# Kernel tuning notes

Measured on AMD Instinct MI355X. Metric: run time of the kernel, lower is better.

## Reference

```python
import jax, jax.numpy as jnp
import numpy as np

B, S, D, H = 4, 2048, 1024, 16
HD = D // H  # 64

def setup_inputs() -> dict:
    key = jax.random.key(0)
    ks = jax.random.split(key, 6)
    scale = 1.0 / np.sqrt(D)
    return {
        "x": jax.random.normal(ks[0], (B, S, D), dtype=jnp.float32),
        "Wq": jax.random.normal(ks[1], (D, D), dtype=jnp.float32) * scale,
        "Wk": jax.random.normal(ks[2], (D, D), dtype=jnp.float32) * scale,
        "Wv": jax.random.normal(ks[3], (D, D), dtype=jnp.float32) * scale,
        "Wo": jax.random.normal(ks[4], (D, D), dtype=jnp.float32) * scale,
        "bo": jnp.zeros((D,), dtype=jnp.float32),
    }

def reference(x, Wq, Wk, Wv, Wo, bo):
    b, s, d = x.shape
    # projections (no bias for q/k/v, matching QKV_BIAS=False)
    q = (x @ Wq).reshape(b, s, H, HD).transpose(0, 2, 1, 3)  # [b,h,s,hd]
    k = (x @ Wk).reshape(b, s, H, HD).transpose(0, 2, 1, 3)
    v = (x @ Wv).reshape(b, s, H, HD).transpose(0, 2, 1, 3)
    scores = jnp.einsum('bhqd,bhkd->bhqk', q, k)  # [b,h,s,s]
    causal = jnp.tril(jnp.ones((s, s), dtype=bool))  # True where allowed
    scores = jnp.where(causal, scores, -jnp.inf)
    attn = jax.nn.softmax(scores / np.sqrt(HD), axis=-1)
    ctx = jnp.einsum('bhqk,bhkd->bhqd', attn, v)  # [b,h,s,hd]
    ctx = ctx.transpose(0, 2, 1, 3).reshape(b, s, d)
    return ctx @ Wo + bo
```

## Files before the change

### kernel.cpp

```cpp
#include <hip/hip_runtime.h>

#define BSZ 4
#define SEQ 2048
#define DIM 1024
#define NH  16
#define HD  64
#define QT  128
#define KT  64
#define PAD 72

typedef float v4f __attribute__((ext_vector_type(4)));
typedef short s8v __attribute__((ext_vector_type(8)));
typedef unsigned short u16;
typedef unsigned short u16x8 __attribute__((ext_vector_type(8)));
typedef unsigned short u16x4 __attribute__((ext_vector_type(4)));
typedef unsigned int u32;

__device__ __forceinline__ u16 f2bf(float f) {
  u32 u = __builtin_bit_cast(u32, f);
  u32 r = u + 0x7fffu + ((u >> 16) & 1u);
  return (u16)(r >> 16);
}
__device__ __forceinline__ float bf2f(u16 h) {
  return __builtin_bit_cast(float, (u32)h << 16);
}
__device__ __forceinline__ float fast_exp2(float x) {
#if __has_builtin(__builtin_amdgcn_exp2f)
  return __builtin_amdgcn_exp2f(x);
#else
  return exp2f(x);
#endif
}
__device__ __forceinline__ void gll16(const u16* g, u16* l) {
  __builtin_amdgcn_global_load_lds((const __attribute__((address_space(1))) void*)g,
                                   (__attribute__((address_space(3))) void*)l, 16, 0, 0);
}
__device__ __forceinline__ void wg_barrier() { asm volatile("s_barrier" ::: "memory"); }
#define WAITCNT_VM4 0xF74
#define WAITCNT_VM0 0xF70

__global__ __launch_bounds__(256) void cast_bf16_kernel(const float* __restrict__ x,
                                                        u16* __restrict__ o, int n4) {
  int i = blockIdx.x * 256 + threadIdx.x;
  if (i >= n4) return;
  v4f v = reinterpret_cast<const v4f*>(x)[i];
  u16x4 r;
  #pragma unroll
  for (int c = 0; c < 4; c++) r[c] = f2bf(v[c]);
  reinterpret_cast<u16x4*>(o)[i] = r;
}

__global__ __launch_bounds__(256) void transpose_cast_kernel(const float* __restrict__ W0,
                                                             const float* __restrict__ W1,
                                                             const float* __restrict__ W2,
                                                             const float* __restrict__ W3,
                                                             u16* __restrict__ out) {
  const float* W = blockIdx.z == 0 ? W0 : blockIdx.z == 1 ? W1 : blockIdx.z == 2 ? W2 : W3;
  const float scale = (blockIdx.z == 0) ? 0.18033688011112042f : 1.0f;
  u16* T = out + (size_t)blockIdx.z * DIM * DIM;
  __shared__ float tile[32][33];
  int tx = threadIdx.x & 31, ty = threadIdx.x >> 5;
  int bn = blockIdx.x * 32, bk = blockIdx.y * 32;
  #pragma unroll
  for (int r = 0; r < 4; r++) {
    int k = bk + ty + r * 8;
    tile[ty + r * 8][tx] = W[(size_t)k * DIM + bn + tx];
  }
  __syncthreads();
  #pragma unroll
  for (int r = 0; r < 4; r++) {
    int n = bn + ty + r * 8;
    T[(size_t)n * DIM + bk + tx] = f2bf(tile[tx][ty + r * 8] * scale);
  }
}


#define STAGE(s, kofs)                                                            \
  gll16(Ag0 + (kofs), Aw0 + (s) * 4096); gll16(Ag1 + (kofs), Aw1 + (s) * 4096);   \
  gll16(Bg0 + (kofs), Bw0 + (s) * 4096); gll16(Bg1 + (kofs), Bw1 + (s) * 4096);

#define COMPUTE(s)                                                                \
  { s8v af[4], bfv[4];                                                            \
    _Pragma("unroll") for (int i = 0; i < 4; i++)                                 \
      af[i] = *(const s8v*)(Al + (s) * 4096 + abase + i * 512);                   \
    _Pragma("unroll") for (int j = 0; j < 4; j++)                                 \
      bfv[j] = *(const s8v*)(Bl + (s) * 4096 + bbase + j * 512);                  \
    _Pragma("unroll") for (int i = 0; i < 4; i++)                                 \
      _Pragma("unroll") for (int j = 0; j < 4; j++)                               \
        acc[i][j] = __builtin_amdgcn_mfma_f32_16x16x32_bf16(af[i], bfv[j],        \
                                                            acc[i][j], 0, 0, 0); }

#define PIPE_STEP(s, nbuf, knext)                                                 \
  __builtin_amdgcn_s_waitcnt(WAITCNT_VM4);                                        \
  wg_barrier();                                                                   \
  STAGE(nbuf, knext)                                                              \
  COMPUTE(s)

#define GEMM_SETUP_AND_LOOP()                                                     \
  const int flat = blockIdx.x + 8 * blockIdx.y;                                   \
  const int xcd = flat & 7, slot = flat >> 3;                                     \
  const int m0 = (xcd * 8 + (slot & 7)) * 128;                                    \
  const int n0 = (slot >> 3) * 128;                                               \
  const int t = threadIdx.x;                                                      \
  const int lane = t & 63, w = t >> 6;                                            \
  const int waveM = w >> 1, waveN = w & 1;                                        \
  const int quad = lane >> 4, l16 = lane & 15;                                    \
  __shared__ u16 Al[12288];                                                       \
  __shared__ u16 Bl[12288];                                                       \
  v4f acc[4][4];                                                                  \
  _Pragma("unroll") for (int i = 0; i < 4; i++)                                   \
    _Pragma("unroll") for (int j = 0; j < 4; j++)                                 \
      acc[i][j] = (v4f){0.f, 0.f, 0.f, 0.f};                                      \
  const int sR = lane & 15, sC = lane >> 4;                                       \
  const u16* Ag0 = A  + (size_t)(m0 + (w * 2 + 0) * 16 + sR) * DIM + sC * 8;      \
  const u16* Ag1 = A  + (size_t)(m0 + (w * 2 + 1) * 16 + sR) * DIM + sC * 8;      \
  const u16* Bg0 = Bt + (size_t)(n0 + (w * 2 + 0) * 16 + sR) * DIM + sC * 8;      \
  const u16* Bg1 = Bt + (size_t)(n0 + (w * 2 + 1) * 16 + sR) * DIM + sC * 8;      \
  u16* Aw0 = Al + (w * 2 + 0) * 512;                                              \
  u16* Aw1 = Al + (w * 2 + 1) * 512;                                              \
  u16* Bw0 = Bl + (w * 2 + 0) * 512;                                              \
  u16* Bw1 = Bl + (w * 2 + 1) * 512;                                              \
  const int abase = waveM * 2048 + quad * 128 + l16 * 8;                          \
  const int bbase = waveN * 2048 + quad * 128 + l16 * 8;                          \
  STAGE(0, 0)                                                                     \
  STAGE(1, 32)                                                                    \
  for (int i3 = 0; i3 < 10; i3++) {                                               \
    const int kb = i3 * 96;                                                       \
    PIPE_STEP(0, 2, kb + 64)                                                      \
    PIPE_STEP(1, 0, kb + 96)                                                      \
    PIPE_STEP(2, 1, kb + 128)                                                     \
  }                                                                               \
  __builtin_amdgcn_s_waitcnt(WAITCNT_VM4);                                        \
  wg_barrier();                                                                   \
  COMPUTE(0)                                                                      \
  __builtin_amdgcn_s_waitcnt(WAITCNT_VM0);                                        \
  wg_barrier();                                                                   \
  COMPUTE(1)

__global__ __launch_bounds__(256, 3) void gemm_qkv(const u16* __restrict__ A, const u16* __restrict__ Wt,
                                                   u16* __restrict__ Qb, u16* __restrict__ Kb,
                                                   u16* __restrict__ Vtg) {
  const int z = blockIdx.z;
  const u16* Bt = Wt + (size_t)z * DIM * DIM;
  GEMM_SETUP_AND_LOOP()
  if (z == 2) {
    #pragma unroll
    for (int i = 0; i < 4; i++) {
      #pragma unroll
      for (int j = 0; j < 4; j++) {
        int gm0 = m0 + waveM * 64 + i * 16 + quad * 4;
        int gn = n0 + waveN * 64 + j * 16 + l16;
        int b = gm0 >> 11, s0 = gm0 & (SEQ - 1), hh = gn >> 6, d = gn & (HD - 1);
        u16x4 o;
        #pragma unroll
        for (int r = 0; r < 4; r++) o[r] = f2bf(acc[i][j][r]);
        *(u16x4*)(Vtg + ((size_t)(b * NH + hh) * HD + d) * SEQ + s0) = o;
      }
    }
  } else {
    u16* C = (z == 0) ? Qb : Kb;
    #pragma unroll
    for (int i = 0; i < 4; i++) {
      #pragma unroll
      for (int j = 0; j < 4; j++) {
        int gn = n0 + waveN * 64 + j * 16 + l16;
        #pragma unroll
        for (int r = 0; r < 4; r++) {
          int gm = m0 + waveM * 64 + i * 16 + quad * 4 + r;
          C[(size_t)gm * DIM + gn] = f2bf(acc[i][j][r]);
        }
      }
    }
  }
}

__global__ __launch_bounds__(256, 3) void gemm_proj(const u16* __restrict__ A, const u16* __restrict__ Bt,
                                                    float* __restrict__ Cf, const float* __restrict__ bias) {
  GEMM_SETUP_AND_LOOP()
  #pragma unroll
  for (int i = 0; i < 4; i++) {
    #pragma unroll
    for (int j = 0; j < 4; j++) {
      int gn = n0 + waveN * 64 + j * 16 + l16;
      float bv = bias[gn];
      #pragma unroll
      for (int r = 0; r < 4; r++) {
        int gm = m0 + waveM * 64 + i * 16 + quad * 4 + r;
        Cf[(size_t)gm * DIM + gn] = acc[i][j][r] + bv;
      }
    }
  }
}

__global__ __launch_bounds__(256, 3) void flash_attn_mfma(const u16* __restrict__ Qb,
                                                          const u16* __restrict__ Kb,
                                                          const u16* __restrict__ Vtg,
                                                          u16* __restrict__ Ob) {
  const int h = blockIdx.x, px = blockIdx.y, bb = blockIdx.z;
  const int t = threadIdx.x;
  const int lane = t & 63, w = t >> 6;
  const int quad = lane >> 4, l16 = lane & 15;

  __shared__ u16 QPs[QT * PAD];
  __shared__ u16 Ks[KT * PAD];
  __shared__ u16 Vs[HD * PAD];

  const size_t qkbase = (size_t)bb * SEQ * DIM + h * HD;
  const size_t vbase = ((size_t)bb * NH + h) * (size_t)HD * SEQ;

  const int vrow = t >> 2, scol = (t & 3) * 16;
  const int krow = ((vrow >> 5) + 2 * ((vrow >> 2) & 1)) * 16 + ((vrow >> 3) & 3) * 4 + (vrow & 3);

  for (int pass = 0; pass < 2; pass++) {
    const int qi = (pass == 0) ? px : (SEQ / QT - 1 - px);
    const int q0 = qi * QT;
    const int wq = q0 + w * 32;
    const int ntiles = 2 * qi + 2;

    __syncthreads();

    {
      const int r = t >> 1, c0 = (t & 1) * 32;
      const u16* src = Qb + qkbase + (size_t)(q0 + r) * DIM + c0;
      #pragma unroll
      for (int ch = 0; ch < 4; ch++)
        *(u16x8*)(QPs + r * PAD + c0 + ch * 8) = *(const u16x8*)(src + ch * 8);
    }
    __syncthreads();

    s8v qf[2][2];
    #pragma unroll
    for (int ni = 0; ni < 2; ni++)
      #pragma unroll
      for (int kc = 0; kc < 2; kc++)
        qf[ni][kc] = *(const s8v*)(QPs + (w * 32 + ni * 16 + l16) * PAD + kc * 32 + quad * 8);

    u16x8 kr0, kr1, vr0, vr1;
    {
      const u16* kp = Kb + qkbase + (size_t)vrow * DIM + scol;
      kr0 = *(const u16x8*)kp; kr1 = *(const u16x8*)(kp + 8);
      const u16* vp = Vtg + vbase + (size_t)vrow * SEQ + scol;
      vr0 = *(const u16x8*)vp; vr1 = *(const u16x8*)(vp + 8);
    }

    float mrun[2] = {-1e30f, -1e30f}, lrun[2] = {0.f, 0.f};
    v4f O[4][2];
    #pragma unroll
    for (int di = 0; di < 4; di++)
      #pragma unroll
      for (int ni = 0; ni < 2; ni++) O[di][ni] = (v4f){0.f, 0.f, 0.f, 0.f};

    for (int it = 0; it < ntiles; ++it) {
      const int kv0 = it * KT;
      __syncthreads();
      *(u16x8*)(Ks + krow * PAD + scol) = kr0;
      *(u16x8*)(Ks + krow * PAD + scol + 8) = kr1;
      *(u16x8*)(Vs + vrow * PAD + scol) = vr0;
      *(u16x8*)(Vs + vrow * PAD + scol + 8) = vr1;
      __syncthreads();
      if (it + 1 < ntiles) {
        const int nkv = kv0 + KT;
        const u16* kp = Kb + qkbase + (size_t)(nkv + vrow) * DIM + scol;
        kr0 = *(const u16x8*)kp; kr1 = *(const u16x8*)(kp + 8);
        const u16* vp = Vtg + vbase + (size_t)vrow * SEQ + nkv + scol;
        vr0 = *(const u16x8*)vp; vr1 = *(const u16x8*)(vp + 8);
      }
      if (kv0 > wq + 31) continue;

      v4f sc[4][2];
      #pragma unroll
      for (int mi = 0; mi < 4; mi++)
        #pragma unroll
        for (int ni = 0; ni < 2; ni++) sc[mi][ni] = (v4f){0.f, 0.f, 0.f, 0.f};
      #pragma unroll
      for (int kc = 0; kc < 2; kc++) {
        #pragma unroll
        for (int mi = 0; mi < 4; mi++) {
          s8v kf = *(const s8v*)(Ks + (mi * 16 + l16) * PAD + kc * 32 + quad * 8);
          sc[mi][0] = __builtin_amdgcn_mfma_f32_16x16x32_bf16(kf, qf[0][kc], sc[mi][0], 0, 0, 0);
          sc[mi][1] = __builtin_amdgcn_mfma_f32_16x16x32_bf16(kf, qf[1][kc], sc[mi][1], 0, 0, 0);
        }
      }

      if (kv0 + KT > wq) {
        #pragma unroll
        for (int mi = 0; mi < 4; mi++) {
          const int kvb = kv0 + (mi & 1) * 32 + quad * 8 + (mi >> 1) * 4;
          #pragma unroll
          for (int ni = 0; ni < 2; ni++) {
            const int qg = wq + ni * 16 + l16;
            #pragma unroll
            for (int r = 0; r < 4; r++)
              if (kvb + r > qg) sc[mi][ni][r] = -1e30f;
          }
        }
      }

      float alpha[2];
      #pragma unroll
      for (int ni = 0; ni < 2; ni++) {
        float mx = -1e30f;
        #pragma unroll
        for (int mi = 0; mi < 4; mi++)
          #pragma unroll
          for (int r = 0; r < 4; r++) mx = fmaxf(mx, sc[mi][ni][r]);
        mx = fmaxf(mx, __shfl_xor(mx, 16, 64));
        mx = fmaxf(mx, __shfl_xor(mx, 32, 64));
        const float mnew = fmaxf(mrun[ni], mx);
        alpha[ni] = fast_exp2(mrun[ni] - mnew);
        mrun[ni] = mnew;
        float rsum = 0.f;
        #pragma unroll
        for (int mi = 0; mi < 4; mi++)
          #pragma unroll
          for (int r = 0; r < 4; r++) {
            float p = fast_exp2(sc[mi][ni][r] - mnew);
            sc[mi][ni][r] = p;
            rsum += p;
          }
        rsum += __shfl_xor(rsum, 16, 64);
        rsum += __shfl_xor(rsum, 32, 64);
        lrun[ni] = lrun[ni] * alpha[ni] + rsum;
      }
      #pragma unroll
      for (int di = 0; di < 4; di++)
        #pragma unroll
        for (int ni = 0; ni < 2; ni++)
          #pragma unroll
          for (int r = 0; r < 4; r++) O[di][ni][r] *= alpha[ni];

      s8v pf[2][2];
      #pragma unroll
      for (int ni = 0; ni < 2; ni++)
        #pragma unroll
        for (int kc = 0; kc < 2; kc++)
          #pragma unroll
          for (int j = 0; j < 8; j++)
            pf[ni][kc][j] = (short)f2bf(sc[kc + 2 * (j >> 2)][ni][j & 3]);

      #pragma unroll
      for (int kc = 0; kc < 2; kc++) {
        #pragma unroll
        for (int di = 0; di < 4; di++) {
          s8v vf = *(const s8v*)(Vs + (di * 16 + l16) * PAD + kc * 32 + quad * 8);
          O[di][0] = __builtin_amdgcn_mfma_f32_16x16x32_bf16(vf, pf[0][kc], O[di][0], 0, 0, 0);
          O[di][1] = __builtin_amdgcn_mfma_f32_16x16x32_bf16(vf, pf[1][kc], O[di][1], 0, 0, 0);
        }
      }
    }

    const float inv0 = 1.f / lrun[0], inv1 = 1.f / lrun[1];
    #pragma unroll
    for (int di = 0; di < 4; di++)
      #pragma unroll
      for (int ni = 0; ni < 2; ni++) {
        const float inv = ni ? inv1 : inv0;
        #pragma unroll
        for (int r = 0; r < 4; r++)
          QPs[(w * 32 + ni * 16 + l16) * PAD + di * 16 + quad * 4 + r] = f2bf(O[di][ni][r] * inv);
      }
    __syncthreads();
    {
      const int r = t >> 1, c0 = (t & 1) * 32;
      u16* dst = Ob + qkbase + (size_t)(q0 + r) * DIM + c0;
      #pragma unroll
      for (int ch = 0; ch < 4; ch++)
        *(u16x8*)(dst + ch * 8) = *(const u16x8*)(QPs + r * PAD + c0 + ch * 8);
    }
  }
}

extern "C" void kernel_launch(void* const* d_in, const int* in_sizes, int n_in,
                              void* d_out, int out_size, void* d_ws, size_t ws_size,
                              hipStream_t stream) {
  (void)in_sizes; (void)n_in; (void)out_size; (void)ws_size;
  const float* x  = (const float*)d_in[0];
  const float* Wq = (const float*)d_in[1];
  const float* Wk = (const float*)d_in[2];
  const float* Wv = (const float*)d_in[3];
  const float* Wo = (const float*)d_in[4];
  const float* bo = (const float*)d_in[5];
  float* out = (float*)d_out;

  char* ws = (char*)d_ws;
  const size_t MB = 1024ull * 1024ull;
  u16* Xb  = (u16*)(ws);
  u16* Wt  = (u16*)(ws + 16 * MB);
  u16* Qb  = (u16*)(ws + 24 * MB);
  u16* Kb  = (u16*)(ws + 40 * MB);
  u16* Vtg = (u16*)(ws + 56 * MB);
  u16* Cb  = (u16*)(ws + 72 * MB);

  const int NTOK = BSZ * SEQ;
  const int n4 = NTOK * DIM / 4;
  cast_bf16_kernel<<<(n4 + 255) / 256, 256, 0, stream>>>(x, Xb, n4);
  transpose_cast_kernel<<<dim3(32, 32, 4), 256, 0, stream>>>(Wq, Wk, Wv, Wo, Wt);

  gemm_qkv<<<dim3(DIM / 128, NTOK / 128, 3), 256, 0, stream>>>(Xb, Wt, Qb, Kb, Vtg);

  flash_attn_mfma<<<dim3(NH, SEQ / QT / 2, BSZ), 256, 0, stream>>>(Qb, Kb, Vtg, Cb);

  gemm_proj<<<dim3(DIM / 128, NTOK / 128), 256, 0, stream>>>(Cb, Wt + 3ull * DIM * DIM, out, bo);
}
```

Before: 303.4 us.

## Switch QKV and output GEMMs to 256x256 tiles with 8-wave phased pipeline

Replaces the 128x128, 4-wave GEMM with a 256x256, 512-thread kernel using 128KB of dynamic LDS. Loads are double-buffered over 64-wide K tiles and split into four phases, each interleaving one global-to-LDS stage with MFMA work, with s_setprio around the MFMA bursts. The launch becomes a 1D grid with an XCD-aware swizzle. The aim is higher arithmetic intensity per LDS byte and fewer blocks. The cost is more barriers per K step, and the projection GEMM launches only 128 blocks, which can underfill the GPU.

```diff
diff --git a/kernel.cpp b/kernel.cpp
--- a/kernel.cpp
+++ b/kernel.cpp
@@ -8,6 +8,7 @@
 #define QT  128
 #define KT  64
 #define PAD 72
+#define NKT (DIM / 64)
 
 typedef float v4f __attribute__((ext_vector_type(4)));
 typedef short s8v __attribute__((ext_vector_type(8)));
@@ -36,8 +37,9 @@
                                    (__attribute__((address_space(3))) void*)l, 16, 0, 0);
 }
 __device__ __forceinline__ void wg_barrier() { asm volatile("s_barrier" ::: "memory"); }
-#define WAITCNT_VM4 0xF74
-#define WAITCNT_VM0 0xF70
+#define WAITCNT_VM4   0xF74
+#define WAITCNT_VM0   0xF70
+#define WAITCNT_LGKM0 0xC07F
 
 __global__ __launch_bounds__(256) void cast_bf16_kernel(const float* __restrict__ x,
                                                         u16* __restrict__ o, int n4) {
@@ -75,118 +77,133 @@
 }
 
 
-#define STAGE(s, kofs)                                                            \
-  gll16(Ag0 + (kofs), Aw0 + (s) * 4096); gll16(Ag1 + (kofs), Aw1 + (s) * 4096);   \
-  gll16(Bg0 + (kofs), Bw0 + (s) * 4096); gll16(Bg1 + (kofs), Bw1 + (s) * 4096);
-
-#define COMPUTE(s)                                                                \
-  { s8v af[4], bfv[4];                                                            \
-    _Pragma("unroll") for (int i = 0; i < 4; i++)                                 \
-      af[i] = *(const s8v*)(Al + (s) * 4096 + abase + i * 512);                   \
+#define ST_A(t_, kc_)                                                             \
+  gll16(Ag0 + (t_) * 64 + (kc_) * 32, Aw0 + ((t_)&1) * 16384 + (kc_) * 8192);     \
+  gll16(Ag1 + (t_) * 64 + (kc_) * 32, Aw1 + ((t_)&1) * 16384 + (kc_) * 8192);
+#define ST_B(t_, kc_)                                                             \
+  gll16(Bg0 + (t_) * 64 + (kc_) * 32, Bw0 + ((t_)&1) * 16384 + (kc_) * 8192);     \
+  gll16(Bg1 + (t_) * 64 + (kc_) * 32, Bw1 + ((t_)&1) * 16384 + (kc_) * 8192);
+
+#define PH(t_, kc_, mh_, STAGES, TAILW)                                           \
+  { const u16* Ab = AL + ((t_)&1) * 16384 + (kc_) * 8192 + aRd;                   \
+    const u16* Bb = BL + ((t_)&1) * 16384 + (kc_) * 8192 + bRd;                   \
+    s8v af[4], bf[4];                                                             \
+    _Pragma("unroll") for (int i_ = 0; i_ < 4; i_++)                              \
+      af[i_] = *(const s8v*)(Ab + ((mh_) * 4 + i_) * 512);                        \
+    _Pragma("unroll") for (int j_ = 0; j_ < 4; j_++)                              \
+      bf[j_] = *(const s8v*)(Bb + j_ * 512);                                      \
+    STAGES                                                                        \
+    wg_barrier();                                                                 \
+    __builtin_amdgcn_s_waitcnt(WAITCNT_LGKM0);                                    \
+    __builtin_amdgcn_s_setprio(1);                                                \
+    _Pragma("unroll") for (int i_ = 0; i_ < 4; i_++)                              \
+      _Pragma("unroll") for (int j_ = 0; j_ < 4; j_++)                            \
+        acc[(mh_) * 4 + i_][j_] = __builtin_amdgcn_mfma_f32_16x16x32_bf16(        \
+            af[i_], bf[j_], acc[(mh_) * 4 + i_][j_], 0, 0, 0);                    \
+    __builtin_amdgcn_s_setprio(0);                                                \
+    TAILW                                                                         \
+    wg_barrier(); }
+
+#define GEMM256_CORE()                                                            \
+  extern __shared__ __align__(16) u16 lds[];                                      \
+  const int t = threadIdx.x;                                                      \
+  const int lane = t & 63, w = t >> 6;                                            \
+  const int waveM = w >> 2, waveN = w & 3;                                        \
+  const int quad = lane >> 4, l16 = lane & 15;                                    \
+  const int sR = lane & 15, sC = lane >> 4;                                       \
+  u16* AL = lds;                                                                  \
+  u16* BL = lds + 32768;                                                          \
+  v4f acc[8][4];                                                                  \
+  _Pragma("unroll") for (int i = 0; i < 8; i++)                                   \
     _Pragma("unroll") for (int j = 0; j < 4; j++)                                 \
-      bfv[j] = *(const s8v*)(Bl + (s) * 4096 + bbase + j * 512);                  \
-    _Pragma("unroll") for (int i = 0; i < 4; i++)                                 \
-      _Pragma("unroll") for (int j = 0; j < 4; j++)                               \
-        acc[i][j] = __builtin_amdgcn_mfma_f32_16x16x32_bf16(af[i], bfv[j],        \
-                                                            acc[i][j], 0, 0, 0); }
-
-#define PIPE_STEP(s, nbuf, knext)                                                 \
+      acc[i][j] = (v4f){0.f, 0.f, 0.f, 0.f};                                      \
+  const u16* Ag0 = A + (size_t)(m0 + w * 32 + sR) * DIM + sC * 8;                 \
+  const u16* Ag1 = A + (size_t)(m0 + w * 32 + 16 + sR) * DIM + sC * 8;            \
+  const u16* Bg0 = Bt + (size_t)(n0 + w * 32 + sR) * DIM + sC * 8;                \
+  const u16* Bg1 = Bt + (size_t)(n0 + w * 32 + 16 + sR) * DIM + sC * 8;           \
+  u16* Aw0 = AL + (w * 2 + 0) * 512;                                              \
+  u16* Aw1 = AL + (w * 2 + 1) * 512;                                              \
+  u16* Bw0 = BL + (w * 2 + 0) * 512;                                              \
+  u16* Bw1 = BL + (w * 2 + 1) * 512;                                              \
+  const int aRd = waveM * 4096 + quad * 128 + l16 * 8;                            \
+  const int bRd = waveN * 2048 + quad * 128 + l16 * 8;                            \
+  ST_A(0, 0) ST_B(0, 0) ST_A(0, 1) ST_B(0, 1) ST_A(1, 0) ST_B(1, 0)              \
   __builtin_amdgcn_s_waitcnt(WAITCNT_VM4);                                        \
   wg_barrier();                                                                   \
-  STAGE(nbuf, knext)                                                              \
-  COMPUTE(s)
-
-#define GEMM_SETUP_AND_LOOP()                                                     \
-  const int flat = blockIdx.x + 8 * blockIdx.y;                                   \
-  const int xcd = flat & 7, slot = flat >> 3;                                     \
-  const int m0 = (xcd * 8 + (slot & 7)) * 128;                                    \
-  const int n0 = (slot >> 3) * 128;                                               \
-  const int t = threadIdx.x;                                                      \
-  const int lane = t & 63, w = t >> 6;                                            \
-  const int waveM = w >> 1, waveN = w & 1;                                        \
-  const int quad = lane >> 4, l16 = lane & 15;                                    \
-  __shared__ u16 Al[12288];                                                       \
-  __shared__ u16 Bl[12288];                                                       \
-  v4f acc[4][4];                                                                  \
-  _Pragma("unroll") for (int i = 0; i < 4; i++)                                   \
-    _Pragma("unroll") for (int j = 0; j < 4; j++)                                 \
-      acc[i][j] = (v4f){0.f, 0.f, 0.f, 0.f};                                      \
-  const int sR = lane & 15, sC = lane >> 4;                                       \
-  const u16* Ag0 = A  + (size_t)(m0 + (w * 2 + 0) * 16 + sR) * DIM + sC * 8;      \
-  const u16* Ag1 = A  + (size_t)(m0 + (w * 2 + 1) * 16 + sR) * DIM + sC * 8;      \
-  const u16* Bg0 = Bt + (size_t)(n0 + (w * 2 + 0) * 16 + sR) * DIM + sC * 8;      \
-  const u16* Bg1 = Bt + (size_t)(n0 + (w * 2 + 1) * 16 + sR) * DIM + sC * 8;      \
-  u16* Aw0 = Al + (w * 2 + 0) * 512;                                              \
-  u16* Aw1 = Al + (w * 2 + 1) * 512;                                              \
-  u16* Bw0 = Bl + (w * 2 + 0) * 512;                                              \
-  u16* Bw1 = Bl + (w * 2 + 1) * 512;                                              \
-  const int abase = waveM * 2048 + quad * 128 + l16 * 8;                          \
-  const int bbase = waveN * 2048 + quad * 128 + l16 * 8;                          \
-  STAGE(0, 0)                                                                     \
-  STAGE(1, 32)                                                                    \
-  for (int i3 = 0; i3 < 10; i3++) {                                               \
-    const int kb = i3 * 96;                                                       \
-    PIPE_STEP(0, 2, kb + 64)                                                      \
-    PIPE_STEP(1, 0, kb + 96)                                                      \
-    PIPE_STEP(2, 1, kb + 128)                                                     \
+  _Pragma("unroll 2") for (int kt = 0; kt < NKT - 2; kt++) {                      \
+    PH(kt, 0, 0, ST_A(kt + 1, 1), )                                               \
+    PH(kt, 0, 1, ST_B(kt + 1, 1), )                                               \
+    PH(kt, 1, 0, ST_A(kt + 2, 0), )                                               \
+    PH(kt, 1, 1, ST_B(kt + 2, 0), __builtin_amdgcn_s_waitcnt(WAITCNT_VM4);)       \
   }                                                                               \
-  __builtin_amdgcn_s_waitcnt(WAITCNT_VM4);                                        \
-  wg_barrier();                                                                   \
-  COMPUTE(0)                                                                      \
-  __builtin_amdgcn_s_waitcnt(WAITCNT_VM0);                                        \
-  wg_barrier();                                                                   \
-  COMPUTE(1)
-
-__global__ __launch_bounds__(256, 3) void gemm_qkv(const u16* __restrict__ A, const u16* __restrict__ Wt,
+  PH(NKT - 2, 0, 0, ST_A(NKT - 1, 1), )                                           \
+  PH(NKT - 2, 0, 1, ST_B(NKT - 1, 1), )                                           \
+  PH(NKT - 2, 1, 0, , )                                                           \
+  PH(NKT - 2, 1, 1, , __builtin_amdgcn_s_waitcnt(WAITCNT_VM0);)                   \
+  PH(NKT - 1, 0, 0, , )                                                           \
+  PH(NKT - 1, 0, 1, , )                                                           \
+  PH(NKT - 1, 1, 0, , )                                                           \
+  PH(NKT - 1, 1, 1, , )
+
+__global__ __launch_bounds__(512, 2) void gemm_qkv(const u16* __restrict__ A, const u16* __restrict__ Wt,
                                                    u16* __restrict__ Qb, u16* __restrict__ Kb,
                                                    u16* __restrict__ Vtg) {
-  const int z = blockIdx.z;
+  const int bid = blockIdx.x;
+  const int swz = (bid & 7) * 48 + (bid >> 3);
+  const int z = swz >> 7;
+  const int rem = swz & 127;
+  const int m0 = (rem >> 2) * 256;
+  const int n0 = (rem & 3) * 256;
   const u16* Bt = Wt + (size_t)z * DIM * DIM;
-  GEMM_SETUP_AND_LOOP()
+  GEMM256_CORE()
   if (z == 2) {
     #pragma unroll
-    for (int i = 0; i < 4; i++) {
-      #pragma unroll
-      for (int j = 0; j < 4; j++) {
-        int gm0 = m0 + waveM * 64 + i * 16 + quad * 4;
-        int gn = n0 + waveN * 64 + j * 16 + l16;
+    for (int mi = 0; mi < 8; mi++) {
+      #pragma unroll
+      for (int ni = 0; ni < 4; ni++) {
+        int gm0 = m0 + waveM * 128 + mi * 16 + quad * 4;
+        int gn = n0 + waveN * 64 + ni * 16 + l16;
         int b = gm0 >> 11, s0 = gm0 & (SEQ - 1), hh = gn >> 6, d = gn & (HD - 1);
         u16x4 o;
         #pragma unroll
-        for (int r = 0; r < 4; r++) o[r] = f2bf(acc[i][j][r]);
+        for (int r = 0; r < 4; r++) o[r] = f2bf(acc[mi][ni][r]);
         *(u16x4*)(Vtg + ((size_t)(b * NH + hh) * HD + d) * SEQ + s0) = o;
       }
     }
   } else {
     u16* C = (z == 0) ? Qb : Kb;
     #pragma unroll
-    for (int i = 0; i < 4; i++) {
-      #pragma unroll
-      for (int j = 0; j < 4; j++) {
-        int gn = n0 + waveN * 64 + j * 16 + l16;
+    for (int mi = 0; mi < 8; mi++) {
+      #pragma unroll
+      for (int ni = 0; ni < 4; ni++) {
+        int gn = n0 + waveN * 64 + ni * 16 + l16;
         #pragma unroll
         for (int r = 0; r < 4; r++) {
-          int gm = m0 + waveM * 64 + i * 16 + quad * 4 + r;
-          C[(size_t)gm * DIM + gn] = f2bf(acc[i][j][r]);
+          int gm = m0 + waveM * 128 + mi * 16 + quad * 4 + r;
+          C[(size_t)gm * DIM + gn] = f2bf(acc[mi][ni][r]);
         }
       }
     }
   }
 }
 
-__global__ __launch_bounds__(256, 3) void gemm_proj(const u16* __restrict__ A, const u16* __restrict__ Bt,
+__global__ __launch_bounds__(512, 2) void gemm_proj(const u16* __restrict__ A, const u16* __restrict__ Bt,
                                                     float* __restrict__ Cf, const float* __restrict__ bias) {
-  GEMM_SETUP_AND_LOOP()
+  const int bid = blockIdx.x;
+  const int swz = (bid & 7) * 16 + (bid >> 3);
+  const int m0 = (swz >> 2) * 256;
+  const int n0 = (swz & 3) * 256;
+  GEMM256_CORE()
   #pragma unroll
-  for (int i = 0; i < 4; i++) {
-    #pragma unroll
-    for (int j = 0; j < 4; j++) {
-      int gn = n0 + waveN * 64 + j * 16 + l16;
-      float bv = bias[gn];
+  for (int ni = 0; ni < 4; ni++) {
+    int gn = n0 + waveN * 64 + ni * 16 + l16;
+    float bv = bias[gn];
+    #pragma unroll
+    for (int mi = 0; mi < 8; mi++) {
       #pragma unroll
       for (int r = 0; r < 4; r++) {
-        int gm = m0 + waveM * 64 + i * 16 + quad * 4 + r;
-        Cf[(size_t)gm * DIM + gn] = acc[i][j][r] + bv;
+        int gm = m0 + waveM * 128 + mi * 16 + quad * 4 + r;
+        Cf[(size_t)gm * DIM + gn] = acc[mi][ni][r] + bv;
       }
     }
   }
@@ -382,6 +399,15 @@
   const float* bo = (const float*)d_in[5];
   float* out = (float*)d_out;
 
+  static bool lds_attr_done = false;
+  if (!lds_attr_done) {
+    hipFuncSetAttribute(reinterpret_cast<const void*>(gemm_qkv),
+                        hipFuncAttributeMaxDynamicSharedMemorySize, 131072);
+    hipFuncSetAttribute(reinterpret_cast<const void*>(gemm_proj),
+                        hipFuncAttributeMaxDynamicSharedMemorySize, 131072);
+    lds_attr_done = true;
+  }
+
   char* ws = (char*)d_ws;
   const size_t MB = 1024ull * 1024ull;
   u16* Xb  = (u16*)(ws);
@@ -396,9 +422,9 @@
   cast_bf16_kernel<<<(n4 + 255) / 256, 256, 0, stream>>>(x, Xb, n4);
   transpose_cast_kernel<<<dim3(32, 32, 4), 256, 0, stream>>>(Wq, Wk, Wv, Wo, Wt);
 
-  gemm_qkv<<<dim3(DIM / 128, NTOK / 128, 3), 256, 0, stream>>>(Xb, Wt, Qb, Kb, Vtg);
+  gemm_qkv<<<dim3(384), 512, 131072, stream>>>(Xb, Wt, Qb, Kb, Vtg);
 
   flash_attn_mfma<<<dim3(NH, SEQ / QT / 2, BSZ), 256, 0, stream>>>(Qb, Kb, Vtg, Cb);
 
-  gemm_proj<<<dim3(DIM / 128, NTOK / 128), 256, 0, stream>>>(Cb, Wt + 3ull * DIM * DIM, out, bo);
-}
+  gemm_proj<<<dim3(128), 512, 131072, stream>>>(Cb, Wt + 3ull * DIM * DIM, out, bo);
+}
```

Result: faster. 284.4 us (-6.2%).
